# Kernel tuning notes

Hardware: AMD Instinct MI355X
Metric: run time of the kernel (lower is better)

The kernel has to match this reference:

```python
import jax, jax.numpy as jnp
import numpy as np

NEG = -1.0e30  # stand-in for -inf, safe under logaddexp in fp32
DEN_SCALE = 1.0


def _ctc_forward(logp, targets, in_lens, tgt_lens):
    """Log-semiring forward (tot score) over the numerator lattice:
    CTC topology composed with the linear target FSA. logp: [B,T,C] (blank=0),
    targets: [B,U] in [1, C-1]. Returns [B] numerator log-scores."""
    B, T, C = logp.shape
    U = targets.shape[1]
    S = 2 * U + 1  # extended label sequence: blank-interleaved
    ext = jnp.zeros((B, S), dtype=jnp.int32).at[:, 1::2].set(targets.astype(jnp.int32))
    # skip transition s-2 -> s allowed only for non-blank, non-repeated labels
    skip_ok = jnp.concatenate(
        [jnp.zeros((B, 2), dtype=bool), (ext[:, 2:] != 0) & (ext[:, 2:] != ext[:, :-2])],
        axis=1,
    )
    emit0 = jnp.take_along_axis(logp[:, 0], ext, axis=1)  # [B,S]
    alpha = jnp.full((B, S), NEG, dtype=logp.dtype)
    alpha = alpha.at[:, 0].set(emit0[:, 0]).at[:, 1].set(emit0[:, 1])
    logp_t = jnp.swapaxes(logp, 0, 1)  # [T,B,C]

    def step(alpha, xs):
        t, lp = xs
        a1 = jnp.concatenate([jnp.full((B, 1), NEG, alpha.dtype), alpha[:, :-1]], axis=1)
        a2 = jnp.concatenate([jnp.full((B, 2), NEG, alpha.dtype), alpha[:, :-2]], axis=1)
        cand = jnp.logaddexp(jnp.logaddexp(alpha, a1), jnp.where(skip_ok, a2, NEG))
        new = cand + jnp.take_along_axis(lp, ext, axis=1)
        alpha = jnp.where((t < in_lens)[:, None], new, alpha)  # freeze past utterance end
        return alpha, None

    alpha, _ = jax.lax.scan(step, alpha, (jnp.arange(1, T), logp_t[1:]))
    last = (2 * tgt_lens).astype(jnp.int32)  # final states: last blank / last label
    a_last = jnp.take_along_axis(alpha, last[:, None], axis=1)[:, 0]
    a_prev = jnp.take_along_axis(alpha, (last - 1)[:, None], axis=1)[:, 0]
    return jnp.logaddexp(a_last, a_prev)


def _den_forward(logp, trans, start, in_lens):
    """Log-semiring forward over the dense denominator graph (bigram token LM):
    states = token classes, transition log-weights trans[C,C]. Returns [B]."""
    B, T, C = logp.shape
    alpha = start[None, :] + logp[:, 0]  # [B,C]
    logp_t = jnp.swapaxes(logp, 0, 1)  # [T,B,C]

    def step(alpha, xs):
        t, lp = xs
        new = jax.nn.logsumexp(alpha[:, :, None] + trans[None], axis=1) + lp
        alpha = jnp.where((t < in_lens)[:, None], new, alpha)
        return alpha, None

    alpha, _ = jax.lax.scan(step, alpha, (jnp.arange(1, T), logp_t[1:]))
    return jax.nn.logsumexp(alpha, axis=1)


def setup_inputs() -> dict:
    key = jax.random.key(0)
    ks = jax.random.split(key, 6)
    B, T, C, U = 32, 2000, 256, 200
    log_probs = jax.nn.log_softmax(jax.random.normal(ks[0], (B, T, C), dtype=jnp.float32), axis=-1)
    targets = jax.random.randint(ks[1], (B, U), 1, C)
    input_lengths = jax.random.randint(ks[2], (B,), T // 2, T + 1)
    target_lengths = jax.random.randint(ks[3], (B,), U // 2, U + 1)
    den_transitions = jax.random.normal(ks[4], (C, C), dtype=jnp.float32) * 0.1
    den_start = jax.random.normal(ks[5], (C,), dtype=jnp.float32) * 0.1
    return {
        "log_probs": log_probs,
        "targets": targets,
        "input_lengths": input_lengths,
        "target_lengths": target_lengths,
        "den_transitions": den_transitions,
        "den_start": den_start,
    }


def reference(log_probs, targets, input_lengths, target_lengths, den_transitions, den_start):
    logp = jax.nn.log_softmax(log_probs, axis=-1)  # idempotent if already normalized
    B, T, C = logp.shape
    U = targets.shape[1]
    in_lens = jnp.clip(input_lengths, 2 * U + 1, T).astype(jnp.int32)
    tgt_lens = jnp.clip(target_lengths, 1, U).astype(jnp.int32)
    tgt = jnp.clip(targets, 1, C - 1)  # blank=0 excluded from targets
    num = _ctc_forward(logp, tgt, in_lens, tgt_lens)
    den = _den_forward(logp, den_transitions, den_start, in_lens)
    tot = num - DEN_SCALE * den  # LF-MMI per-utterance objective
    valid = tot > 0.5 * NEG  # mimic get_tot_objf_and_num_frames -inf filtering
    n = jnp.maximum(jnp.sum(valid), 1)
    return -jnp.sum(jnp.where(valid, tot, 0.0)) / n
```

## Files before the change

kernel.cpp:

```cpp
#include <hip/hip_runtime.h>
#include <stdint.h>
#include <stddef.h>

#define NEGF (-1.0e30f)

typedef __attribute__((ext_vector_type(2))) _Float16 half2_t;

constexpr int Bn = 32;
constexpr int Tn = 2000;
constexpr int Cn = 256;
constexpr int Un = 200;
constexpr int Sn = 2 * Un + 1;
constexpr float Kn = 4096.0f;

__device__ __forceinline__ float fdot2f(uint32_t a, uint32_t b, float c) {
  half2_t ha = __builtin_bit_cast(half2_t, a);
  half2_t hb = __builtin_bit_cast(half2_t, b);
#if __has_builtin(__builtin_amdgcn_fdot2)
  return __builtin_amdgcn_fdot2(ha, hb, c, false);
#else
  return c + (float)ha.x * (float)hb.x + (float)ha.y * (float)hb.y;
#endif
}

__device__ __forceinline__ float quad_sum(float x) {
#if __has_builtin(__builtin_amdgcn_update_dpp)
  int xi = __builtin_bit_cast(int, x);
  int y = __builtin_amdgcn_update_dpp(0, xi, 0xB1, 0xF, 0xF, false);
  float s = x + __builtin_bit_cast(float, y);
  int si = __builtin_bit_cast(int, s);
  int z = __builtin_amdgcn_update_dpp(0, si, 0x4E, 0xF, 0xF, false);
  return s + __builtin_bit_cast(float, z);
#else
  x += __shfl_xor(x, 1, 64);
  x += __shfl_xor(x, 2, 64);
  return x;
#endif
}

__device__ __forceinline__ float lse3(float a, float b, float c) {
  float m = fmaxf(fmaxf(a, b), c);
  return m + __logf(__expf(a - m) + __expf(b - m) + __expf(c - m));
}

__device__ __forceinline__ int clampi(int v, int lo, int hi) {
  return v < lo ? lo : (v > hi ? hi : v);
}

__global__ __launch_bounds__(256)
__attribute__((amdgpu_waves_per_eu(1, 1)))
void fwd_kernel(
    const float* __restrict__ logp, const int* __restrict__ targets,
    const int* __restrict__ in_lens, const int* __restrict__ tgt_lens,
    const float* __restrict__ trans, const float* __restrict__ start,
    float* __restrict__ ws) {
  const int tid = threadIdx.x;
  const int bid = blockIdx.x;

  if (bid < Bn) {
    const int b = bid;
    const int L = clampi(in_lens[b], Sn, Tn);
    const int q = tid & 3;
    const int u = tid >> 2;
    const int jw = u + 64 * q;

    __shared__ __align__(16) _Float16 eaH[2][Cn];
    __shared__ float sred[4];

    uint32_t Ereg[4][32];
#pragma unroll
    for (int k = 0; k < 4; ++k) {
      const int jk = u + 64 * k;
#pragma unroll
      for (int m = 0; m < 32; ++m) {
        const int i0 = 64 * q + 2 * m;
        float e0 = __expf(trans[i0 * Cn + jk]);
        float e1 = __expf(trans[(i0 + 1) * Cn + jk]);
        half2_t h;
        h.x = (_Float16)e0;
        h.y = (_Float16)e1;
        Ereg[k][m] = __builtin_bit_cast(uint32_t, h);
      }
    }

    const float* lpb = logp + (size_t)b * Tn * Cn;

    float G = -__logf(Kn);
    eaH[0][jw] = (_Float16)(Kn * __expf(start[jw] + lpb[jw]));
    float lp_next = lpb[Cn + jw];
    __syncthreads();

    const uint32_t ONE2 = 0x3C003C00u;

    for (int t = 1; t < L; ++t) {
      const int pr = (t - 1) & 1, pw = t & 1;
      const float lp_cur = lp_next;
      const int tnext = (t + 1 < L) ? t + 1 : L - 1;
      lp_next = lpb[(size_t)tnext * Cn + jw];
      const float p = __expf(lp_cur);

      const uint4* eap = (const uint4*)(&eaH[pr][64 * q]);
      float a0 = 0.f, a1 = 0.f, a2 = 0.f, a3 = 0.f, zz = 0.f;
#pragma unroll
      for (int m4 = 0; m4 < 8; ++m4) {
        const uint4 e4 = eap[m4];
        a0 = fdot2f(Ereg[0][4 * m4 + 0], e4.x, a0);
        a0 = fdot2f(Ereg[0][4 * m4 + 1], e4.y, a0);
        a0 = fdot2f(Ereg[0][4 * m4 + 2], e4.z, a0);
        a0 = fdot2f(Ereg[0][4 * m4 + 3], e4.w, a0);
        a1 = fdot2f(Ereg[1][4 * m4 + 0], e4.x, a1);
        a1 = fdot2f(Ereg[1][4 * m4 + 1], e4.y, a1);
        a1 = fdot2f(Ereg[1][4 * m4 + 2], e4.z, a1);
        a1 = fdot2f(Ereg[1][4 * m4 + 3], e4.w, a1);
        a2 = fdot2f(Ereg[2][4 * m4 + 0], e4.x, a2);
        a2 = fdot2f(Ereg[2][4 * m4 + 1], e4.y, a2);
        a2 = fdot2f(Ereg[2][4 * m4 + 2], e4.z, a2);
        a2 = fdot2f(Ereg[2][4 * m4 + 3], e4.w, a2);
        a3 = fdot2f(Ereg[3][4 * m4 + 0], e4.x, a3);
        a3 = fdot2f(Ereg[3][4 * m4 + 1], e4.y, a3);
        a3 = fdot2f(Ereg[3][4 * m4 + 2], e4.z, a3);
        a3 = fdot2f(Ereg[3][4 * m4 + 3], e4.w, a3);
        zz = fdot2f(ONE2, e4.x, zz);
        zz = fdot2f(ONE2, e4.y, zz);
        zz = fdot2f(ONE2, e4.z, zz);
        zz = fdot2f(ONE2, e4.w, zz);
      }
      a0 = quad_sum(a0);
      a1 = quad_sum(a1);
      a2 = quad_sum(a2);
      a3 = quad_sum(a3);
      zz = quad_sum(zz);

      const float s = (q == 0) ? a0 : (q == 1) ? a1 : (q == 2) ? a2 : a3;
      const float invZ = Kn * __frcp_rn(zz);
      G -= __logf(invZ);
      eaH[pw][jw] = (_Float16)(s * p * invZ);
      __syncthreads();
    }

    {
      const int pL = (L - 1) & 1;
      float e = (float)eaH[pL][tid];
#pragma unroll
      for (int off = 32; off >= 1; off >>= 1) e += __shfl_xor(e, off, 64);
      const int lane = tid & 63, wid = tid >> 6;
      if (lane == 0) sred[wid] = e;
      __syncthreads();
      if (tid == 0) {
        float ssum = (sred[0] + sred[1]) + (sred[2] + sred[3]);
        ws[Bn + b] = G + __logf(ssum);
      }
    }
  } else {
    const int b = bid - Bn;
    const int L = clampi(in_lens[b], Sn, Tn);
    const int tl = clampi(tgt_lens[b], 1, Un);

    __shared__ float abuf[2][Sn + 3];
    const float* lpb = logp + (size_t)b * Tn * Cn;
    const int* tgtb = targets + b * Un;

    const int s1 = tid;
    const int s2 = tid + 256;
    int e1 = 0, e2 = 0;
    bool k1 = false, k2 = false;
    if (s1 & 1) {
      const int uu = (s1 - 1) >> 1;
      e1 = clampi(tgtb[uu], 1, Cn - 1);
      if (uu > 0) k1 = (e1 != clampi(tgtb[uu - 1], 1, Cn - 1));
    }
    if ((s2 < Sn) && (s2 & 1)) {
      const int uu = (s2 - 1) >> 1;
      e2 = clampi(tgtb[uu], 1, Cn - 1);
      k2 = (e2 != clampi(tgtb[uu - 1], 1, Cn - 1));
    }

    abuf[0][s1 + 2] = (s1 == 0) ? lpb[0] : (s1 == 1 ? lpb[e1] : NEGF);
    if (s2 < Sn) abuf[0][s2 + 2] = NEGF;
    if (tid < 2) { abuf[0][tid] = NEGF; abuf[1][tid] = NEGF; }
    float pe1 = lpb[Cn + e1];
    float pe2 = lpb[Cn + e2];
    __syncthreads();

    int cur = 0;
    for (int t = 1; t < L; ++t) {
      const float em1 = pe1, em2 = pe2;
      const int tnext = (t + 1 < L) ? t + 1 : L - 1;
      pe1 = lpb[(size_t)tnext * Cn + e1];
      pe2 = lpb[(size_t)tnext * Cn + e2];
      const float* A = abuf[cur];
      float* Bv = abuf[cur ^ 1];
      {
        const float x = A[s1 + 2], y = A[s1 + 1];
        const float z = k1 ? A[s1] : NEGF;
        Bv[s1 + 2] = lse3(x, y, z) + em1;
      }
      if (s2 < Sn) {
        const float x = A[s2 + 2], y = A[s2 + 1];
        const float z = k2 ? A[s2] : NEGF;
        Bv[s2 + 2] = lse3(x, y, z) + em2;
      }
      __syncthreads();
      cur ^= 1;
    }
    if (tid == 0) {
      const int l = 2 * tl;
      const float x = abuf[cur][l + 2], y = abuf[cur][l + 1];
      const float m = fmaxf(x, y);
      ws[b] = m + __logf(__expf(x - m) + __expf(y - m));
    }
  }
}

__global__ void finalize_kernel(const float* __restrict__ ws,
                                float* __restrict__ out) {
  const int tid = threadIdx.x;
  float tot = 0.f, cnt = 0.f;
  if (tid < Bn) {
    const float tv = ws[tid] - ws[Bn + tid];
    const bool valid = tv > 0.5f * NEGF;
    tot = valid ? tv : 0.f;
    cnt = valid ? 1.f : 0.f;
  }
#pragma unroll
  for (int off = 32; off >= 1; off >>= 1) {
    tot += __shfl_xor(tot, off, 64);
    cnt += __shfl_xor(cnt, off, 64);
  }
  if (tid == 0) out[0] = -tot / fmaxf(cnt, 1.f);
}

extern "C" void kernel_launch(void* const* d_in, const int* in_sizes, int n_in,
                              void* d_out, int out_size, void* d_ws, size_t ws_size,
                              hipStream_t stream) {
  const float* logp = (const float*)d_in[0];
  const int* targets = (const int*)d_in[1];
  const int* in_lens = (const int*)d_in[2];
  const int* tgt_lens = (const int*)d_in[3];
  const float* trans = (const float*)d_in[4];
  const float* start = (const float*)d_in[5];
  float* ws = (float*)d_ws;
  float* out = (float*)d_out;
  (void)in_sizes; (void)n_in; (void)out_size; (void)ws_size;

  fwd_kernel<<<dim3(2 * Bn), dim3(256), 0, stream>>>(
      logp, targets, in_lens, tgt_lens, trans, start, ws);
  finalize_kernel<<<dim3(1), dim3(64), 0, stream>>>(ws, out);
}
```

Before: 1.222 ms.

## Split denominator matvec across 8 lanes with DPP transpose-reduce and packed-half Z sum

The dense denominator recursion now splits each column's reduction over 8 lanes of 32 source states instead of 4 lanes of 64, holding eight 16-word register columns per thread. The per-lane partial sums are combined with a butterfly of DPP exchanges that halves the number of live accumulators at each stage, rather than fully reducing every column. The normaliser is accumulated with packed half adds before a single dot. The LDS alpha buffer is padded to an 80-byte stride per 32-entry group, apparently to avoid bank conflicts. The goal is shorter serial fdot2 chains per time step. The cost is more cross-lane traffic, and summing Z in half precision risks some accuracy loss.

New measurement: 1.134 ms. 7.2% less time.

```diff
diff --git a/kernel.cpp b/kernel.cpp
--- a/kernel.cpp
+++ b/kernel.cpp
@@ -5,6 +5,7 @@
 #define NEGF (-1.0e30f)
 
 typedef __attribute__((ext_vector_type(2))) _Float16 half2_t;
+typedef uint32_t u32x16 __attribute__((ext_vector_type(16)));
 
 constexpr int Bn = 32;
 constexpr int Tn = 2000;
@@ -23,19 +24,25 @@
 #endif
 }
 
-__device__ __forceinline__ float quad_sum(float x) {
+template <int CTRL>
+__device__ __forceinline__ float dppf(float x) {
 #if __has_builtin(__builtin_amdgcn_update_dpp)
   int xi = __builtin_bit_cast(int, x);
-  int y = __builtin_amdgcn_update_dpp(0, xi, 0xB1, 0xF, 0xF, false);
-  float s = x + __builtin_bit_cast(float, y);
-  int si = __builtin_bit_cast(int, s);
-  int z = __builtin_amdgcn_update_dpp(0, si, 0x4E, 0xF, 0xF, false);
-  return s + __builtin_bit_cast(float, z);
+  int y = __builtin_amdgcn_update_dpp(0, xi, CTRL, 0xF, 0xF, false);
+  return __builtin_bit_cast(float, y);
 #else
-  x += __shfl_xor(x, 1, 64);
-  x += __shfl_xor(x, 2, 64);
   return x;
 #endif
+}
+#define dpp_x1(v) dppf<0xB1>(v)
+#define dpp_x2(v) dppf<0x4E>(v)
+#define dpp_x7(v) dppf<0x141>(v)
+
+__device__ __forceinline__ uint32_t packe(float a, float b) {
+  half2_t h;
+  h.x = (_Float16)a;
+  h.y = (_Float16)b;
+  return __builtin_bit_cast(uint32_t, h);
 }
 
 __device__ __forceinline__ float lse3(float a, float b, float c) {
@@ -60,37 +67,42 @@
   if (bid < Bn) {
     const int b = bid;
     const int L = clampi(in_lens[b], Sn, Tn);
-    const int q = tid & 3;
-    const int u = tid >> 2;
-    const int jw = u + 64 * q;
-
-    __shared__ __align__(16) _Float16 eaH[2][Cn];
+    const int q = tid & 7;
+    const int u = tid >> 3;
+    const int jw = u + 32 * q;
+
+    __shared__ __align__(16) char eaLDS[2 * 8 * 80];
     __shared__ float sred[4];
 
-    uint32_t Ereg[4][32];
-#pragma unroll
-    for (int k = 0; k < 4; ++k) {
-      const int jk = u + 64 * k;
-#pragma unroll
-      for (int m = 0; m < 32; ++m) {
-        const int i0 = 64 * q + 2 * m;
-        float e0 = __expf(trans[i0 * Cn + jk]);
-        float e1 = __expf(trans[(i0 + 1) * Cn + jk]);
-        half2_t h;
-        h.x = (_Float16)e0;
-        h.y = (_Float16)e1;
-        Ereg[k][m] = __builtin_bit_cast(uint32_t, h);
-      }
-    }
+    const float* trow = trans;
+#define EP(c, m) packe(__expf(trow[(32 * q + 2 * (m)) * Cn + (c)]), \
+                       __expf(trow[(32 * q + 2 * (m) + 1) * Cn + (c)]))
+#define MKCOL(c)                                                          \
+  (u32x16){EP(c, 0),  EP(c, 1),  EP(c, 2),  EP(c, 3),  EP(c, 4),          \
+           EP(c, 5),  EP(c, 6),  EP(c, 7),  EP(c, 8),  EP(c, 9),          \
+           EP(c, 10), EP(c, 11), EP(c, 12), EP(c, 13), EP(c, 14), EP(c, 15)}
+    u32x16 E0 = MKCOL(u + 0);
+    u32x16 E1 = MKCOL(u + 32);
+    u32x16 E2 = MKCOL(u + 64);
+    u32x16 E3 = MKCOL(u + 96);
+    u32x16 E4 = MKCOL(u + 128);
+    u32x16 E5 = MKCOL(u + 160);
+    u32x16 E6 = MKCOL(u + 192);
+    u32x16 E7 = MKCOL(u + 224);
+#undef MKCOL
+#undef EP
 
     const float* lpb = logp + (size_t)b * Tn * Cn;
+    const char* rbase0 = eaLDS + 80 * q;
+    char* wptr0 = eaLDS + 80 * q + 2 * u;
 
     float G = -__logf(Kn);
-    eaH[0][jw] = (_Float16)(Kn * __expf(start[jw] + lpb[jw]));
+    *(_Float16*)(wptr0) = (_Float16)(Kn * __expf(start[jw] + lpb[jw]));
     float lp_next = lpb[Cn + jw];
     __syncthreads();
 
     const uint32_t ONE2 = 0x3C003C00u;
+    const bool q4 = (q & 4) != 0, q2 = (q & 2) != 0, q1 = (q & 1) != 0;
 
     for (int t = 1; t < L; ++t) {
       const int pr = (t - 1) & 1, pw = t & 1;
@@ -99,48 +111,60 @@
       lp_next = lpb[(size_t)tnext * Cn + jw];
       const float p = __expf(lp_cur);
 
-      const uint4* eap = (const uint4*)(&eaH[pr][64 * q]);
-      float a0 = 0.f, a1 = 0.f, a2 = 0.f, a3 = 0.f, zz = 0.f;
-#pragma unroll
-      for (int m4 = 0; m4 < 8; ++m4) {
-        const uint4 e4 = eap[m4];
-        a0 = fdot2f(Ereg[0][4 * m4 + 0], e4.x, a0);
-        a0 = fdot2f(Ereg[0][4 * m4 + 1], e4.y, a0);
-        a0 = fdot2f(Ereg[0][4 * m4 + 2], e4.z, a0);
-        a0 = fdot2f(Ereg[0][4 * m4 + 3], e4.w, a0);
-        a1 = fdot2f(Ereg[1][4 * m4 + 0], e4.x, a1);
-        a1 = fdot2f(Ereg[1][4 * m4 + 1], e4.y, a1);
-        a1 = fdot2f(Ereg[1][4 * m4 + 2], e4.z, a1);
-        a1 = fdot2f(Ereg[1][4 * m4 + 3], e4.w, a1);
-        a2 = fdot2f(Ereg[2][4 * m4 + 0], e4.x, a2);
-        a2 = fdot2f(Ereg[2][4 * m4 + 1], e4.y, a2);
-        a2 = fdot2f(Ereg[2][4 * m4 + 2], e4.z, a2);
-        a2 = fdot2f(Ereg[2][4 * m4 + 3], e4.w, a2);
-        a3 = fdot2f(Ereg[3][4 * m4 + 0], e4.x, a3);
-        a3 = fdot2f(Ereg[3][4 * m4 + 1], e4.y, a3);
-        a3 = fdot2f(Ereg[3][4 * m4 + 2], e4.z, a3);
-        a3 = fdot2f(Ereg[3][4 * m4 + 3], e4.w, a3);
-        zz = fdot2f(ONE2, e4.x, zz);
-        zz = fdot2f(ONE2, e4.y, zz);
-        zz = fdot2f(ONE2, e4.z, zz);
-        zz = fdot2f(ONE2, e4.w, zz);
-      }
-      a0 = quad_sum(a0);
-      a1 = quad_sum(a1);
-      a2 = quad_sum(a2);
-      a3 = quad_sum(a3);
-      zz = quad_sum(zz);
-
-      const float s = (q == 0) ? a0 : (q == 1) ? a1 : (q == 2) ? a2 : a3;
-      const float invZ = Kn * __frcp_rn(zz);
+      const uint4* eap = (const uint4*)(rbase0 + pr * 640);
+      float a0 = 0.f, a1 = 0.f, a2 = 0.f, a3 = 0.f;
+      float a4 = 0.f, a5 = 0.f, a6 = 0.f, a7 = 0.f;
+      half2_t zpk = {(_Float16)0.f, (_Float16)0.f};
+#define B2(x) __builtin_bit_cast(half2_t, x)
+#define DOT8(idx, ev)               \
+  a0 = fdot2f(E0[idx], ev, a0);     \
+  a1 = fdot2f(E1[idx], ev, a1);     \
+  a2 = fdot2f(E2[idx], ev, a2);     \
+  a3 = fdot2f(E3[idx], ev, a3);     \
+  a4 = fdot2f(E4[idx], ev, a4);     \
+  a5 = fdot2f(E5[idx], ev, a5);     \
+  a6 = fdot2f(E6[idx], ev, a6);     \
+  a7 = fdot2f(E7[idx], ev, a7);
+#define DOTQ(m4)                                                      \
+  {                                                                   \
+    const uint4 e4 = eap[m4];                                         \
+    DOT8(4 * (m4) + 0, e4.x)                                          \
+    DOT8(4 * (m4) + 1, e4.y)                                          \
+    DOT8(4 * (m4) + 2, e4.z)                                          \
+    DOT8(4 * (m4) + 3, e4.w)                                          \
+    zpk = zpk + ((B2(e4.x) + B2(e4.y)) + (B2(e4.z) + B2(e4.w)));      \
+  }
+      DOTQ(0)
+      DOTQ(1)
+      DOTQ(2)
+      DOTQ(3)
+#undef DOTQ
+#undef DOT8
+
+      float zc = fdot2f(ONE2, __builtin_bit_cast(uint32_t, zpk), 0.f);
+      zc += dpp_x1(zc);
+      zc += dpp_x2(zc);
+      zc += dpp_x7(zc);
+
+      float g, t0, t1, t2, t3, w0, w1, s;
+      g = q4 ? a0 : a4;  t0 = (q4 ? a4 : a0) + dpp_x7(g);
+      g = q4 ? a1 : a5;  t1 = (q4 ? a5 : a1) + dpp_x7(g);
+      g = q4 ? a2 : a6;  t2 = (q4 ? a6 : a2) + dpp_x7(g);
+      g = q4 ? a3 : a7;  t3 = (q4 ? a7 : a3) + dpp_x7(g);
+      g = q2 ? t0 : t2;  w0 = (q2 ? t2 : t0) + dpp_x2(g);
+      g = q2 ? t1 : t3;  w1 = (q2 ? t3 : t1) + dpp_x2(g);
+      g = q1 ? w0 : w1;  s  = (q1 ? w1 : w0) + dpp_x1(g);
+
+      const float invZ = Kn * __frcp_rn(zc);
       G -= __logf(invZ);
-      eaH[pw][jw] = (_Float16)(s * p * invZ);
+      *(_Float16*)(wptr0 + pw * 640) = (_Float16)(s * p * invZ);
       __syncthreads();
     }
 
     {
       const int pL = (L - 1) & 1;
-      float e = (float)eaH[pL][tid];
+      const char* fb = eaLDS + pL * 640;
+      float e = (float)(*(const _Float16*)(fb + 80 * (tid >> 5) + 2 * (tid & 31)));
 #pragma unroll
       for (int off = 32; off >= 1; off >>= 1) e += __shfl_xor(e, off, 64);
       const int lane = tid & 63, wid = tid >> 6;
```
